# Performance work log

Hardware: AMD Instinct MI355X
Metric: run time of the kernel (lower is better)

## Reference

```python
import jax, jax.numpy as jnp
import numpy as np

MODES = 256


def setup_inputs() -> dict:
    key = jax.random.key(0)
    k1, k2, k3, k4, k5 = jax.random.split(key, 5)
    B, C_IN, C_OUT, N, KM = 8, 128, 128, 8192, 32
    scale = 1.0 / (C_IN * C_OUT)
    return {
        "x": jax.random.normal(k1, (B, C_IN, N), dtype=jnp.float32),
        "wbases": jax.random.normal(k2, (B, N, MODES), dtype=jnp.float32),
        "bases": jax.random.normal(k3, (B, N, MODES), dtype=jnp.float32),
        "weights": scale * jax.random.normal(k4, (C_IN, C_OUT, KM), dtype=jnp.float32),
        "D": jax.random.normal(k5, (KM, MODES), dtype=jnp.float32),
    }


def reference(x, wbases, bases, weights, D):
    # Project onto weighted bases: (b, c_in, n) x (b, n, modes) -> (b, c_in, modes)
    x_hat = jnp.einsum('bcx,bxk->bck', x, wbases[:, :, :MODES])
    # D-weighted channel mixing. Original: x_hat1[b,i,j,k] = x_hat[b,i,k]*D[j,k];
    # y[b,o,k] = sum_{i,j} x_hat1[b,i,j,k] * weights[i,o,j]
    # Equivalent fused contraction (same math, no 4D broadcast):
    y_hat = jnp.einsum('bik,jk,ioj->bok', x_hat, D, weights)
    # Reconstruct on output bases: (b, c_out, modes) x (b, n, modes) -> (b, c_out, n)
    y = jnp.einsum('bck,bxk->bcx', y_hat, bases[:, :, :MODES])
    return y
```

## Files before the change

kernel.cpp:

```cpp
#include <hip/hip_runtime.h>

#define B_    8
#define CIN   128
#define COUT  128
#define NX    8192
#define KMJ   32
#define MODES 256

typedef short bf16x8 __attribute__((ext_vector_type(8)));
typedef float f32x4  __attribute__((ext_vector_type(4)));

__device__ __forceinline__ float bf2f(unsigned short u) {
    union { unsigned int i; float f; } v; v.i = ((unsigned int)u) << 16; return v.f;
}
__device__ __forceinline__ unsigned short f2bf(float f) {
    union { float f; unsigned int i; } v; v.f = f;
    unsigned int x = v.i;
    return (unsigned short)((x + 0x7fffu + ((x >> 16) & 1u)) >> 16);
}
__device__ __forceinline__ bf16x8 cvt8(const float* __restrict__ p) {
    f32x4 a = *(const f32x4*)p;
    f32x4 b = *(const f32x4*)(p + 4);
    bf16x8 r;
    r[0] = (short)f2bf(a[0]); r[1] = (short)f2bf(a[1]);
    r[2] = (short)f2bf(a[2]); r[3] = (short)f2bf(a[3]);
    r[4] = (short)f2bf(b[0]); r[5] = (short)f2bf(b[1]);
    r[6] = (short)f2bf(b[2]); r[7] = (short)f2bf(b[3]);
    return r;
}
__device__ __forceinline__ ushort4 cvt4(f32x4 a) {
    ushort4 r;
    r.x = f2bf(a[0]); r.y = f2bf(a[1]); r.z = f2bf(a[2]); r.w = f2bf(a[3]);
    return r;
}

__global__ __launch_bounds__(256) void k1_wk(const float* __restrict__ W,
                                             const float* __restrict__ D,
                                             unsigned short* __restrict__ Wk) {
    int wave = threadIdx.x >> 6, lane = threadIdx.x & 63;
    int quad = lane >> 4, l16 = lane & 15;
    int gw  = blockIdx.x * 4 + wave;
    int oi0 = gw * 16;
    int i0  = oi0 & 127, o0 = oi0 >> 7;
    bf16x8 bfrag = cvt8(W + ((size_t)(i0 + l16) * COUT + o0) * KMJ + quad * 8);
#pragma unroll
    for (int m = 0; m < 4; m++) {
        int k0 = (blockIdx.y * 4 + m) * 16;
        bf16x8 afrag;
#pragma unroll
        for (int jj = 0; jj < 8; jj++)
            afrag[jj] = (short)f2bf(D[(quad * 8 + jj) * MODES + k0 + l16]);
        f32x4 acc = {0.f, 0.f, 0.f, 0.f};
        acc = __builtin_amdgcn_mfma_f32_16x16x32_bf16(afrag, bfrag, acc, 0, 0, 0);
#pragma unroll
        for (int r = 0; r < 4; r++)
            Wk[(size_t)(k0 + quad * 4 + r) * (CIN * COUT) + oi0 + l16] = f2bf(acc[r]);
    }
}

__global__ __launch_bounds__(1024, 8) void k2_xhat(const float* __restrict__ X,
                                                   const float* __restrict__ WB,
                                                   unsigned short* __restrict__ PART) {
    __shared__ __align__(16) unsigned short Xs[128 * 40];
    __shared__ __align__(16) unsigned short WBT[128 * 40];
    int nt = blockIdx.x, b = blockIdx.y, kh = blockIdx.z;
    int r0 = nt * 256;
    int t  = threadIdx.x;
    int wave = t >> 6, lane = t & 63;
    int wm = wave >> 2, wk = wave & 3;
    int quad = lane >> 4, l16 = lane & 15;
    int sw = quad ^ (l16 & 3);

    const float* xb  = X  + (size_t)b * CIN * NX;
    const float* wbb = WB + (size_t)b * NX * MODES + kh * 128;

    bool isX = (t >= 512);
    int j  = t & 511;
    int xr = j >> 2, xseg = j & 3;
    int kq = j >> 4, np = j & 15;

    const float* gx = xb + (size_t)xr * NX + r0 + xseg * 8;
    const float* gw = wbb + (size_t)(r0 + 2 * np) * MODES + 4 * kq;
    unsigned short* xw = Xs + xr * 40 + ((xseg ^ (xr & 3)) << 3);

    f32x4 acc[2][2];
#pragma unroll
    for (int i = 0; i < 2; i++)
#pragma unroll
        for (int jj = 0; jj < 2; jj++) acc[i][jj] = (f32x4){0.f, 0.f, 0.f, 0.f};

    f32x4 st0, st1;
    if (isX) { st0 = *(const f32x4*)gx; st1 = *(const f32x4*)(gx + 4); }
    else     { st0 = *(const f32x4*)gw; st1 = *(const f32x4*)(gw + MODES); }

    for (int p = 0; p < 8; p++) {
        if (p) __syncthreads();
        if (isX) {
            *(ushort4*)xw       = cvt4(st0);
            *(ushort4*)(xw + 4) = cvt4(st1);
        } else {
#pragma unroll
            for (int jj = 0; jj < 4; jj++) {
                int k = 4 * kq + jj;
                unsigned int w = (unsigned int)f2bf(st0[jj]) |
                                 ((unsigned int)f2bf(st1[jj]) << 16);
                *(unsigned int*)(WBT + k * 40 + (((np >> 2) ^ (k & 3)) << 3) + ((np & 3) << 1)) = w;
            }
        }
        __syncthreads();

        if (p < 7) {
            if (isX) { gx += 32;          st0 = *(const f32x4*)gx; st1 = *(const f32x4*)(gx + 4); }
            else     { gw += 32 * MODES;  st0 = *(const f32x4*)gw; st1 = *(const f32x4*)(gw + MODES); }
        }

        bf16x8 af[2], bfv[2];
#pragma unroll
        for (int tm = 0; tm < 2; tm++)
            af[tm] = *(const bf16x8*)(Xs + (wm * 32 + tm * 16 + l16) * 40 + (sw << 3));
#pragma unroll
        for (int tn = 0; tn < 2; tn++)
            bfv[tn] = *(const bf16x8*)(WBT + (wk * 32 + tn * 16 + l16) * 40 + (sw << 3));
#pragma unroll
        for (int tm = 0; tm < 2; tm++)
#pragma unroll
            for (int tn = 0; tn < 2; tn++)
                acc[tm][tn] = __builtin_amdgcn_mfma_f32_16x16x32_bf16(af[tm], bfv[tn], acc[tm][tn], 0, 0, 0);
    }

    unsigned short* pb = PART + ((size_t)b * 32 + nt) * (CIN * MODES) + kh * 128;
#pragma unroll
    for (int tm = 0; tm < 2; tm++) {
        int c = wm * 32 + tm * 16 + quad * 4;
#pragma unroll
        for (int tn = 0; tn < 2; tn++) {
            int km = wk * 32 + tn * 16 + l16;
#pragma unroll
            for (int r = 0; r < 4; r++)
                pb[(size_t)(c + r) * MODES + km] = f2bf(acc[tm][tn][r]);
        }
    }
}

__global__ __launch_bounds__(256) void k2b_red(const unsigned short* __restrict__ PART,
                                               float* __restrict__ XH) {
    int e = blockIdx.x * 256 + threadIdx.x;
    const unsigned short* p = PART + (size_t)(e >> 15) * 32 * (CIN * MODES) + (e & 32767);
    float acc = 0.f;
#pragma unroll
    for (int nt = 0; nt < 32; nt++) acc += bf2f(p[nt * (CIN * MODES)]);
    XH[e] = acc;
}

__global__ __launch_bounds__(256, 2) void k3_yhat(const float* __restrict__ XH,
                                                  const unsigned short* __restrict__ Wk,
                                                  unsigned short* __restrict__ YH) {
    __shared__ float xs[128][8];
    int k = blockIdx.x, oh = blockIdx.y;
    int t = threadIdx.x;
#pragma unroll
    for (int l = 0; l < 4; l++) {
        int e = l * 256 + t;
        int i = e >> 3, bb = e & 7;
        xs[i][bb] = XH[(size_t)bb * (CIN * MODES) + (size_t)i * MODES + k];
    }
    int o = oh * 64 + (t & 63), bq = t >> 6;
    const unsigned short* wp = Wk + (size_t)k * (CIN * COUT) + (size_t)o * CIN;
    bf16x8 wc[16];
#pragma unroll
    for (int ii = 0; ii < 16; ii++)
        wc[ii] = *(const bf16x8*)(wp + ii * 8);
    __syncthreads();
    float a0 = 0.f, a1 = 0.f;
#pragma unroll
    for (int ii = 0; ii < 16; ii++)
#pragma unroll
        for (int jj = 0; jj < 8; jj++) {
            float w = bf2f((unsigned short)wc[ii][jj]);
            int i = ii * 8 + jj;
            a0 += w * xs[i][bq * 2];
            a1 += w * xs[i][bq * 2 + 1];
        }
    YH[((size_t)(bq * 2)     * COUT + o) * MODES + k] = f2bf(a0);
    YH[((size_t)(bq * 2 + 1) * COUT + o) * MODES + k] = f2bf(a1);
}

__global__ __launch_bounds__(1024, 8) void k4_y(const unsigned short* __restrict__ YH,
                                                const float* __restrict__ BA,
                                                float* __restrict__ Y) {
    __shared__ __align__(16) unsigned short As[128 * 40];
    __shared__ __align__(16) unsigned short Bs[128 * 40];
    int b  = blockIdx.y;
    int n0 = blockIdx.x * 128;
    int t  = threadIdx.x;
    int wave = t >> 6, lane = t & 63;
    int wm = wave >> 2, wn = wave & 3;
    int quad = lane >> 4, l16 = lane & 15;
    int sw = quad ^ (l16 & 3);

    const unsigned short* yhb = YH + (size_t)b * COUT * MODES;
    const float* bab = BA + (size_t)b * NX * MODES + (size_t)n0 * MODES;

    bool isA = (t < 512);
    int j  = t & 511;
    int rr = j >> 2, seg = j & 3;
    int ssw = (seg ^ (rr & 3)) << 3;

    const unsigned short* ga = yhb + (size_t)rr * MODES + seg * 8;
    const float* gb = bab + (size_t)rr * MODES + seg * 8;

    f32x4 acc[2][2];
#pragma unroll
    for (int i = 0; i < 2; i++)
#pragma unroll
        for (int jj = 0; jj < 2; jj++) acc[i][jj] = (f32x4){0.f, 0.f, 0.f, 0.f};

    bf16x8 sa; f32x4 sb0, sb1;
    if (isA) sa = *(const bf16x8*)ga;
    else { sb0 = *(const f32x4*)gb; sb1 = *(const f32x4*)(gb + 4); }

    for (int p = 0; p < 8; p++) {
        if (p) __syncthreads();
        if (isA) {
            *(bf16x8*)(As + rr * 40 + ssw) = sa;
        } else {
            bf16x8 v;
            v[0] = (short)f2bf(sb0[0]); v[1] = (short)f2bf(sb0[1]);
            v[2] = (short)f2bf(sb0[2]); v[3] = (short)f2bf(sb0[3]);
            v[4] = (short)f2bf(sb1[0]); v[5] = (short)f2bf(sb1[1]);
            v[6] = (short)f2bf(sb1[2]); v[7] = (short)f2bf(sb1[3]);
            *(bf16x8*)(Bs + rr * 40 + ssw) = v;
        }
        __syncthreads();

        if (p < 7) {
            if (isA) { ga += 32; sa = *(const bf16x8*)ga; }
            else     { gb += 32; sb0 = *(const f32x4*)gb; sb1 = *(const f32x4*)(gb + 4); }
        }

        bf16x8 af[2], bfv[2];
#pragma unroll
        for (int tm = 0; tm < 2; tm++)
            af[tm] = *(const bf16x8*)(As + (wm * 32 + tm * 16 + l16) * 40 + (sw << 3));
#pragma unroll
        for (int tn = 0; tn < 2; tn++)
            bfv[tn] = *(const bf16x8*)(Bs + (wn * 32 + tn * 16 + l16) * 40 + (sw << 3));
#pragma unroll
        for (int tm = 0; tm < 2; tm++)
#pragma unroll
            for (int tn = 0; tn < 2; tn++)
                acc[tm][tn] = __builtin_amdgcn_mfma_f32_16x16x32_bf16(af[tm], bfv[tn], acc[tm][tn], 0, 0, 0);
    }

    float* yb = Y + (size_t)b * COUT * NX;
#pragma unroll
    for (int tm = 0; tm < 2; tm++) {
        int o = wm * 32 + tm * 16 + quad * 4;
#pragma unroll
        for (int tn = 0; tn < 2; tn++) {
            int n = n0 + wn * 32 + tn * 16 + l16;
#pragma unroll
            for (int r = 0; r < 4; r++)
                yb[(size_t)(o + r) * NX + n] = acc[tm][tn][r];
        }
    }
}

extern "C" void kernel_launch(void* const* d_in, const int* in_sizes, int n_in,
                              void* d_out, int out_size, void* d_ws, size_t ws_size,
                              hipStream_t stream) {
    const float* X  = (const float*)d_in[0];
    const float* WB = (const float*)d_in[1];
    const float* BA = (const float*)d_in[2];
    const float* W  = (const float*)d_in[3];
    const float* D  = (const float*)d_in[4];
    float* Y = (float*)d_out;

    char* ws = (char*)d_ws;
    unsigned short* Wk   = (unsigned short*)ws;
    float*          XH   = (float*)(ws + (8u << 20));
    unsigned short* YH   = (unsigned short*)(ws + (9u << 20));
    unsigned short* PART = (unsigned short*)(ws + (10u << 20));

    k1_wk  <<<dim3(256, 4),   256,  0, stream>>>(W, D, Wk);
    k2_xhat<<<dim3(32, 8, 2), 1024, 0, stream>>>(X, WB, PART);
    k2b_red<<<1024,           256,  0, stream>>>(PART, XH);
    k3_yhat<<<dim3(256, 2),   256,  0, stream>>>(XH, Wk, YH);
    k4_y   <<<dim3(64, 8),    1024, 0, stream>>>(YH, BA, Y);
}
```

Before: 219.5 us.

## Halve x_hat split-N partials and transpose reduced x_hat for coalesced k3 loads

The projection kernel now processes 512 rows of N per block instead of 256, halving the number of bf16 partial tiles written and then reduced. The reduction kernel uses vectorized 8-wide bf16 loads and writes x_hat transposed as [mode][b*c_in] through shared memory, so k3 reads one contiguous 1024-float row per mode instead of strided gathers. The trade-off is that the projection kernel launches half as many blocks, 256 in total, which lowers parallelism across CUs. Its launch-bounds occupancy hint also drops from 8 to 4.

```diff
diff --git a/kernel.cpp b/kernel.cpp
--- a/kernel.cpp
+++ b/kernel.cpp
@@ -58,13 +58,13 @@
     }
 }
 
-__global__ __launch_bounds__(1024, 8) void k2_xhat(const float* __restrict__ X,
+__global__ __launch_bounds__(1024, 4) void k2_xhat(const float* __restrict__ X,
                                                    const float* __restrict__ WB,
                                                    unsigned short* __restrict__ PART) {
     __shared__ __align__(16) unsigned short Xs[128 * 40];
     __shared__ __align__(16) unsigned short WBT[128 * 40];
-    int nt = blockIdx.x, b = blockIdx.y, kh = blockIdx.z;
-    int r0 = nt * 256;
+    int np = blockIdx.x, b = blockIdx.y, kh = blockIdx.z;
+    int r0 = np * 512;
     int t  = threadIdx.x;
     int wave = t >> 6, lane = t & 63;
     int wm = wave >> 2, wk = wave & 3;
@@ -77,10 +77,10 @@
     bool isX = (t >= 512);
     int j  = t & 511;
     int xr = j >> 2, xseg = j & 3;
-    int kq = j >> 4, np = j & 15;
+    int kq = j >> 4, nq = j & 15;
 
     const float* gx = xb + (size_t)xr * NX + r0 + xseg * 8;
-    const float* gw = wbb + (size_t)(r0 + 2 * np) * MODES + 4 * kq;
+    const float* gw = wbb + (size_t)(r0 + 2 * nq) * MODES + 4 * kq;
     unsigned short* xw = Xs + xr * 40 + ((xseg ^ (xr & 3)) << 3);
 
     f32x4 acc[2][2];
@@ -93,7 +93,7 @@
     if (isX) { st0 = *(const f32x4*)gx; st1 = *(const f32x4*)(gx + 4); }
     else     { st0 = *(const f32x4*)gw; st1 = *(const f32x4*)(gw + MODES); }
 
-    for (int p = 0; p < 8; p++) {
+    for (int p = 0; p < 16; p++) {
         if (p) __syncthreads();
         if (isX) {
             *(ushort4*)xw       = cvt4(st0);
@@ -104,12 +104,12 @@
                 int k = 4 * kq + jj;
                 unsigned int w = (unsigned int)f2bf(st0[jj]) |
                                  ((unsigned int)f2bf(st1[jj]) << 16);
-                *(unsigned int*)(WBT + k * 40 + (((np >> 2) ^ (k & 3)) << 3) + ((np & 3) << 1)) = w;
+                *(unsigned int*)(WBT + k * 40 + (((nq >> 2) ^ (k & 3)) << 3) + ((nq & 3) << 1)) = w;
             }
         }
         __syncthreads();
 
-        if (p < 7) {
+        if (p < 15) {
             if (isX) { gx += 32;          st0 = *(const f32x4*)gx; st1 = *(const f32x4*)(gx + 4); }
             else     { gw += 32 * MODES;  st0 = *(const f32x4*)gw; st1 = *(const f32x4*)(gw + MODES); }
         }
@@ -128,7 +128,7 @@
                 acc[tm][tn] = __builtin_amdgcn_mfma_f32_16x16x32_bf16(af[tm], bfv[tn], acc[tm][tn], 0, 0, 0);
     }
 
-    unsigned short* pb = PART + ((size_t)b * 32 + nt) * (CIN * MODES) + kh * 128;
+    unsigned short* pb = PART + ((size_t)b * 16 + np) * (CIN * MODES) + kh * 128;
 #pragma unroll
     for (int tm = 0; tm < 2; tm++) {
         int c = wm * 32 + tm * 16 + quad * 4;
@@ -143,16 +143,35 @@
 }
 
 __global__ __launch_bounds__(256) void k2b_red(const unsigned short* __restrict__ PART,
-                                               float* __restrict__ XH) {
-    int e = blockIdx.x * 256 + threadIdx.x;
-    const unsigned short* p = PART + (size_t)(e >> 15) * 32 * (CIN * MODES) + (e & 32767);
-    float acc = 0.f;
-#pragma unroll
-    for (int nt = 0; nt < 32; nt++) acc += bf2f(p[nt * (CIN * MODES)]);
-    XH[e] = acc;
-}
-
-__global__ __launch_bounds__(256, 2) void k3_yhat(const float* __restrict__ XH,
+                                               float* __restrict__ XHT) {
+    __shared__ float xt[8][512];
+    int k0 = blockIdx.x * 8, bh = blockIdx.y;
+    int t = threadIdx.x;
+#pragma unroll
+    for (int q = 0; q < 2; q++) {
+        int bi = bh * 512 + q * 256 + t;
+        float a[8] = {0.f, 0.f, 0.f, 0.f, 0.f, 0.f, 0.f, 0.f};
+        const unsigned short* p = PART + ((size_t)((bi >> 7) * 16) * 128 + (bi & 127)) * MODES + k0;
+#pragma unroll
+        for (int np = 0; np < 16; np++) {
+            bf16x8 v = *(const bf16x8*)p;
+#pragma unroll
+            for (int jj = 0; jj < 8; jj++) a[jj] += bf2f((unsigned short)v[jj]);
+            p += (size_t)128 * MODES;
+        }
+#pragma unroll
+        for (int jj = 0; jj < 8; jj++) xt[jj][q * 256 + t] = a[jj];
+    }
+    __syncthreads();
+#pragma unroll
+    for (int q = 0; q < 4; q++) {
+        int idx = q * 1024 + t * 4;
+        int row = idx >> 9, col = idx & 511;
+        *(f32x4*)(XHT + (size_t)(k0 + row) * 1024 + bh * 512 + col) = *(const f32x4*)&xt[row][col];
+    }
+}
+
+__global__ __launch_bounds__(256, 2) void k3_yhat(const float* __restrict__ XHT,
                                                   const unsigned short* __restrict__ Wk,
                                                   unsigned short* __restrict__ YH) {
     __shared__ float xs[128][8];
@@ -161,8 +180,7 @@
 #pragma unroll
     for (int l = 0; l < 4; l++) {
         int e = l * 256 + t;
-        int i = e >> 3, bb = e & 7;
-        xs[i][bb] = XH[(size_t)bb * (CIN * MODES) + (size_t)i * MODES + k];
+        xs[e & 127][e >> 7] = XHT[(size_t)k * 1024 + e];
     }
     int o = oh * 64 + (t & 63), bq = t >> 6;
     const unsigned short* wp = Wk + (size_t)k * (CIN * COUT) + (size_t)o * CIN;
@@ -278,13 +296,13 @@
 
     char* ws = (char*)d_ws;
     unsigned short* Wk   = (unsigned short*)ws;
-    float*          XH   = (float*)(ws + (8u << 20));
+    float*          XHT  = (float*)(ws + (8u << 20));
     unsigned short* YH   = (unsigned short*)(ws + (9u << 20));
     unsigned short* PART = (unsigned short*)(ws + (10u << 20));
 
     k1_wk  <<<dim3(256, 4),   256,  0, stream>>>(W, D, Wk);
-    k2_xhat<<<dim3(32, 8, 2), 1024, 0, stream>>>(X, WB, PART);
-    k2b_red<<<1024,           256,  0, stream>>>(PART, XH);
-    k3_yhat<<<dim3(256, 2),   256,  0, stream>>>(XH, Wk, YH);
+    k2_xhat<<<dim3(16, 8, 2), 1024, 0, stream>>>(X, WB, PART);
+    k2b_red<<<dim3(32, 2),    256,  0, stream>>>(PART, XHT);
+    k3_yhat<<<dim3(256, 2),   256,  0, stream>>>(XHT, Wk, YH);
     k4_y   <<<dim3(64, 8),    1024, 0, stream>>>(YH, BA, Y);
 }
```

New measurement: 228.1 us. 1.04x slower.
